# Kernel optimization log

Measured on AMD Instinct MI355X. Metric: run time of the kernel, lower is better.

## Reference

```python
import jax, jax.numpy as jnp
import numpy as np

EPS = 1e-06
SIGMA_C = 2.0


def setup_inputs() -> dict:
    key = jax.random.key(0)
    k1, k2 = jax.random.split(key)
    B, L, D, T = 16, 512, 256, 2048
    text = jax.random.normal(k1, (B, L, D), dtype=jnp.float32)
    durs = jax.random.randint(k2, (B, L), 0, 8, dtype=jnp.int64)
    return {"text": text, "durs": durs, "total_time": T}


def reference(text, durs, total_time):
    # text: [B, L, D], durs: [B, L] int, total_time: static python int T
    d = durs.astype(jnp.float32)
    # NOTE: faithful to original: mean = durs/2 + cumsum(durs) (cumsum includes current dur)
    mean = d / 2.0 + jnp.cumsum(d, axis=-1)            # [B, L]
    sigma = d / SIGMA_C + EPS                          # [B, L]
    t = jnp.arange(total_time, dtype=jnp.float32) + 0.5  # [T]
    # Normal pdf evaluated at t: exp(log_prob) = exp(-0.5 z^2) / (sigma * sqrt(2 pi))
    z = (t[None, :, None] - mean[:, None, :]) / sigma[:, None, :]  # [B, T, L]
    inv_norm = 1.0 / (sigma[:, None, :] * jnp.sqrt(2.0 * jnp.pi))
    probs = jnp.exp(-0.5 * z * z) * inv_norm           # [B, T, L]
    probs = probs / (probs.sum(-1, keepdims=True) + EPS)
    return jnp.einsum("btl,bld->btd", probs, text)     # [B, T, D]
```

## Files before the change

### kernel.cpp

```cpp
#include <hip/hip_runtime.h>
#include <math.h>

#define L 512
#define NTHREADS 256
#define BLOCK_TT 32
#define ZWIN 9.0f
#define NXCD 8

typedef __attribute__((ext_vector_type(8))) short bf16x8;
typedef __attribute__((ext_vector_type(4))) float f32x4;

static constexpr float EPS = 1e-6f;
static constexpr float INV_SQRT_2PI = 0.39894228040143267794f;

union BFrag { unsigned int u[4]; bf16x8 h; };

__global__ __launch_bounds__(NTHREADS, 4) void ge_mfma(
    const int*   __restrict__ durs,
    const float* __restrict__ text,
    float*       __restrict__ out,
    int B, int T, int tilesPerB, int nwg)
{
    __shared__ float2 s_mi[L];

    const int tid  = threadIdx.x;
    const int lane = tid & 63;
    const int wid  = tid >> 6;
    const int g    = lane >> 4;
    const int mrow = lane & 15;

    const int orig = blockIdx.x;
    const int wg   = (nwg % NXCD == 0) ? (orig & (NXCD - 1)) * (nwg / NXCD) + (orig >> 3)
                                       : orig;
    const int b      = wg / tilesPerB;
    const int tbase0 = (wg % tilesPerB) * BLOCK_TT;

    const int r0 = lane << 3;
    const int4 da = ((const int4*)(durs + (size_t)b * L + r0))[0];
    const int4 db = ((const int4*)(durs + (size_t)b * L + r0))[1];
    int dv[8] = {da.x, da.y, da.z, da.w, db.x, db.y, db.z, db.w};
    int cs[8];
    int run = 0;
    #pragma unroll
    for (int j = 0; j < 8; ++j) { run += dv[j]; cs[j] = run; }
    int v = run;
    #pragma unroll
    for (int off = 1; off < 64; off <<= 1) {
        int n = __shfl_up(v, off, 64);
        if (lane >= off) v += n;
    }
    const int excl = v - run;

    #pragma unroll
    for (int j = 0; j < 8; ++j) {
        const float d  = (float)dv[j];
        const float m  = (float)(cs[j] + excl) + 0.5f * d;
        const float sg = 0.5f * d + EPS;
        s_mi[r0 + j] = make_float2(m, 1.0f / sg);
    }
    asm volatile("s_waitcnt lgkmcnt(0)" ::: "memory");
    __builtin_amdgcn_sched_barrier(0);

    const float* tbp = text + (size_t)b * L * 256 + (wid << 6) + mrow;

    #pragma unroll
    for (int half = 0; half < 2; ++half) {
        const int t0 = tbase0 + (half << 4);

        const float tlo = (float)t0 + 0.5f, thi = (float)t0 + 15.5f;
        int mn = L, mx = -1;
        #pragma unroll
        for (int j = 0; j < 8; ++j) {
            const float d  = (float)dv[j];
            const float m  = (float)(cs[j] + excl) + 0.5f * d;
            const float sg = 0.5f * d + EPS;
            const float r  = ZWIN * sg;
            if (dv[j] >= 1 && m + r >= tlo && m - r <= thi) {
                mn = min(mn, r0 + j);
                mx = max(mx, r0 + j);
            }
        }
        #pragma unroll
        for (int off = 32; off > 0; off >>= 1) {
            mn = min(mn, __shfl_xor(mn, off, 64));
            mx = max(mx, __shfl_xor(mx, off, 64));
        }

        f32x4 acc0 = {0,0,0,0}, acc1 = {0,0,0,0}, acc2 = {0,0,0,0}, acc3 = {0,0,0,0};
        float psum = 0.f;
        const float tf = (float)(t0 + mrow) + 0.5f;

        for (int kb = (mn & ~7); kb <= mx; kb += 32) {
            const int k0 = kb + (g << 3);

            float p[8];
            #pragma unroll
            for (int j = 0; j < 8; ++j) {
                const int k = k0 + j;
                const float2 mi = s_mi[k & (L - 1)];
                const float u = (tf - mi.x) * mi.y;
                float pj = __expf(-0.5f * u * u) * mi.y * INV_SQRT_2PI;
                pj = (k <= mx) ? pj : 0.f;
                psum += pj;
                p[j] = pj;
            }
            BFrag A;
            #pragma unroll
            for (int w = 0; w < 4; ++w)
                asm("v_cvt_pk_bf16_f32 %0, %1, %2"
                    : "=v"(A.u[w]) : "v"(p[2 * w]), "v"(p[2 * w + 1]));

            BFrag B0, B1, B2, B3;
            #pragma unroll
            for (int jp = 0; jp < 4; ++jp) {
                const int ka = min(k0 + 2 * jp,     L - 1);
                const int kc = min(k0 + 2 * jp + 1, L - 1);
                const float* ra = tbp + (size_t)ka * 256;
                const float* rc = tbp + (size_t)kc * 256;
                const float a0 = ra[0], a1 = ra[16], a2 = ra[32], a3 = ra[48];
                const float c0 = rc[0], c1 = rc[16], c2 = rc[32], c3 = rc[48];
                asm("v_cvt_pk_bf16_f32 %0, %1, %2" : "=v"(B0.u[jp]) : "v"(a0), "v"(c0));
                asm("v_cvt_pk_bf16_f32 %0, %1, %2" : "=v"(B1.u[jp]) : "v"(a1), "v"(c1));
                asm("v_cvt_pk_bf16_f32 %0, %1, %2" : "=v"(B2.u[jp]) : "v"(a2), "v"(c2));
                asm("v_cvt_pk_bf16_f32 %0, %1, %2" : "=v"(B3.u[jp]) : "v"(a3), "v"(c3));
            }

            acc0 = __builtin_amdgcn_mfma_f32_16x16x32_bf16(A.h, B0.h, acc0, 0, 0, 0);
            acc1 = __builtin_amdgcn_mfma_f32_16x16x32_bf16(A.h, B1.h, acc1, 0, 0, 0);
            acc2 = __builtin_amdgcn_mfma_f32_16x16x32_bf16(A.h, B2.h, acc2, 0, 0, 0);
            acc3 = __builtin_amdgcn_mfma_f32_16x16x32_bf16(A.h, B3.h, acc3, 0, 0, 0);
        }

        psum += __shfl_xor(psum, 16, 64);
        psum += __shfl_xor(psum, 32, 64);
        const float rn = 1.0f / (psum + EPS);

        const int trow = g << 2;
        const float rr0 = __shfl(rn, trow + 0, 64);
        const float rr1 = __shfl(rn, trow + 1, 64);
        const float rr2 = __shfl(rn, trow + 2, 64);
        const float rr3 = __shfl(rn, trow + 3, 64);

        float* ob = out + ((size_t)b * T + t0 + trow) * 256 + (wid << 6) + mrow;
        if (t0 + trow + 3 < T) {
            ob[0*256 +  0] = acc0[0] * rr0;  ob[1*256 +  0] = acc0[1] * rr1;
            ob[2*256 +  0] = acc0[2] * rr2;  ob[3*256 +  0] = acc0[3] * rr3;
            ob[0*256 + 16] = acc1[0] * rr0;  ob[1*256 + 16] = acc1[1] * rr1;
            ob[2*256 + 16] = acc1[2] * rr2;  ob[3*256 + 16] = acc1[3] * rr3;
            ob[0*256 + 32] = acc2[0] * rr0;  ob[1*256 + 32] = acc2[1] * rr1;
            ob[2*256 + 32] = acc2[2] * rr2;  ob[3*256 + 32] = acc2[3] * rr3;
            ob[0*256 + 48] = acc3[0] * rr0;  ob[1*256 + 48] = acc3[1] * rr1;
            ob[2*256 + 48] = acc3[2] * rr2;  ob[3*256 + 48] = acc3[3] * rr3;
        }
    }
}

extern "C" void kernel_launch(void* const* d_in, const int* in_sizes, int n_in,
                              void* d_out, int out_size, void* d_ws, size_t ws_size,
                              hipStream_t stream) {
    const int*   durs = (const int*)d_in[1];
    const float* text = (const float*)d_in[0];
    float*       out  = (float*)d_out;

    const int BL = in_sizes[1];
    const int D  = in_sizes[0] / BL;
    const int B  = BL / L;
    const int T  = out_size / (B * D);
    const int tilesPerB = (T + BLOCK_TT - 1) / BLOCK_TT;
    const int nwg = B * tilesPerB;

    ge_mfma<<<dim3(nwg), dim3(NTHREADS), 0, stream>>>(durs, text, out, B, T, tilesPerB, nwg);
}
```

Before: 15.24 us.

## Merge the two 16-row halves into one K loop sharing text fragments

Instead of two separate K loops (one per 16-row half of the 32-row time tile), the kernel computes the active K window once for the whole tile and runs a single loop. Each iteration builds two probability fragments and reuses one set of loaded and converted text B fragments for 8 MFMAs. This halves the global loads and bf16 conversions of text per tile and removes a loop's overhead. In exchange it raises accumulator register pressure, and the K window is the union over both halves, so some extra zero-weight work is done.

Result: faster. 14.84 us (-2.6%).

```diff
diff --git a/kernel.cpp b/kernel.cpp
--- a/kernel.cpp
+++ b/kernel.cpp
@@ -51,106 +51,118 @@
     }
     const int excl = v - run;
 
+    const float tlo = (float)tbase0 + 0.5f;
+    const float thi = (float)tbase0 + (float)BLOCK_TT - 0.5f;
+    int mn = L, mx = -1;
     #pragma unroll
     for (int j = 0; j < 8; ++j) {
         const float d  = (float)dv[j];
         const float m  = (float)(cs[j] + excl) + 0.5f * d;
         const float sg = 0.5f * d + EPS;
         s_mi[r0 + j] = make_float2(m, 1.0f / sg);
+        const float r = ZWIN * sg;
+        if (dv[j] >= 1 && m + r >= tlo && m - r <= thi) {
+            mn = min(mn, r0 + j);
+            mx = max(mx, r0 + j);
+        }
+    }
+    #pragma unroll
+    for (int off = 32; off > 0; off >>= 1) {
+        mn = min(mn, __shfl_xor(mn, off, 64));
+        mx = max(mx, __shfl_xor(mx, off, 64));
     }
     asm volatile("s_waitcnt lgkmcnt(0)" ::: "memory");
     __builtin_amdgcn_sched_barrier(0);
 
+    f32x4 a00 = {0,0,0,0}, a01 = {0,0,0,0}, a02 = {0,0,0,0}, a03 = {0,0,0,0};
+    f32x4 a10 = {0,0,0,0}, a11 = {0,0,0,0}, a12 = {0,0,0,0}, a13 = {0,0,0,0};
+    float psum0 = 0.f, psum1 = 0.f;
+    const float tf0 = (float)(tbase0 + mrow) + 0.5f;
+    const float tf1 = tf0 + 16.f;
     const float* tbp = text + (size_t)b * L * 256 + (wid << 6) + mrow;
 
+    for (int kb = (mn & ~7); kb <= mx; kb += 32) {
+        const int k0 = kb + (g << 3);
+
+        BFrag A0, A1;
+        #pragma unroll
+        for (int jp = 0; jp < 4; ++jp) {
+            const int ka = k0 + 2 * jp;
+            const int kc = ka + 1;
+            const float2 mia = s_mi[ka & (L - 1)];
+            const float2 mic = s_mi[kc & (L - 1)];
+            const float ca = mia.y * INV_SQRT_2PI;
+            const float cc = mic.y * INV_SQRT_2PI;
+            const float u0a = (tf0 - mia.x) * mia.y;
+            const float u0c = (tf0 - mic.x) * mic.y;
+            const float u1a = (tf1 - mia.x) * mia.y;
+            const float u1c = (tf1 - mic.x) * mic.y;
+            float p0a = __expf(-0.5f * u0a * u0a) * ca;
+            float p0c = __expf(-0.5f * u0c * u0c) * cc;
+            float p1a = __expf(-0.5f * u1a * u1a) * ca;
+            float p1c = __expf(-0.5f * u1c * u1c) * cc;
+            p0a = (ka <= mx) ? p0a : 0.f;  p1a = (ka <= mx) ? p1a : 0.f;
+            p0c = (kc <= mx) ? p0c : 0.f;  p1c = (kc <= mx) ? p1c : 0.f;
+            psum0 += p0a + p0c;
+            psum1 += p1a + p1c;
+            asm("v_cvt_pk_bf16_f32 %0, %1, %2" : "=v"(A0.u[jp]) : "v"(p0a), "v"(p0c));
+            asm("v_cvt_pk_bf16_f32 %0, %1, %2" : "=v"(A1.u[jp]) : "v"(p1a), "v"(p1c));
+        }
+
+        BFrag B0, B1, B2, B3;
+        #pragma unroll
+        for (int jp = 0; jp < 4; ++jp) {
+            const int ka = min(k0 + 2 * jp,     L - 1);
+            const int kc = min(k0 + 2 * jp + 1, L - 1);
+            const float* ra = tbp + (size_t)ka * 256;
+            const float* rc = tbp + (size_t)kc * 256;
+            const float b0 = ra[0], b1 = ra[16], b2 = ra[32], b3 = ra[48];
+            const float c0 = rc[0], c1 = rc[16], c2 = rc[32], c3 = rc[48];
+            asm("v_cvt_pk_bf16_f32 %0, %1, %2" : "=v"(B0.u[jp]) : "v"(b0), "v"(c0));
+            asm("v_cvt_pk_bf16_f32 %0, %1, %2" : "=v"(B1.u[jp]) : "v"(b1), "v"(c1));
+            asm("v_cvt_pk_bf16_f32 %0, %1, %2" : "=v"(B2.u[jp]) : "v"(b2), "v"(c2));
+            asm("v_cvt_pk_bf16_f32 %0, %1, %2" : "=v"(B3.u[jp]) : "v"(b3), "v"(c3));
+        }
+
+        a00 = __builtin_amdgcn_mfma_f32_16x16x32_bf16(A0.h, B0.h, a00, 0, 0, 0);
+        a01 = __builtin_amdgcn_mfma_f32_16x16x32_bf16(A0.h, B1.h, a01, 0, 0, 0);
+        a02 = __builtin_amdgcn_mfma_f32_16x16x32_bf16(A0.h, B2.h, a02, 0, 0, 0);
+        a03 = __builtin_amdgcn_mfma_f32_16x16x32_bf16(A0.h, B3.h, a03, 0, 0, 0);
+        a10 = __builtin_amdgcn_mfma_f32_16x16x32_bf16(A1.h, B0.h, a10, 0, 0, 0);
+        a11 = __builtin_amdgcn_mfma_f32_16x16x32_bf16(A1.h, B1.h, a11, 0, 0, 0);
+        a12 = __builtin_amdgcn_mfma_f32_16x16x32_bf16(A1.h, B2.h, a12, 0, 0, 0);
+        a13 = __builtin_amdgcn_mfma_f32_16x16x32_bf16(A1.h, B3.h, a13, 0, 0, 0);
+    }
+
+    const int trow = g << 2;
     #pragma unroll
     for (int half = 0; half < 2; ++half) {
-        const int t0 = tbase0 + (half << 4);
+        float ps = half ? psum1 : psum0;
+        ps += __shfl_xor(ps, 16, 64);
+        ps += __shfl_xor(ps, 32, 64);
+        const float rn = 1.0f / (ps + EPS);
 
-        const float tlo = (float)t0 + 0.5f, thi = (float)t0 + 15.5f;
-        int mn = L, mx = -1;
-        #pragma unroll
-        for (int j = 0; j < 8; ++j) {
-            const float d  = (float)dv[j];
-            const float m  = (float)(cs[j] + excl) + 0.5f * d;
-            const float sg = 0.5f * d + EPS;
-            const float r  = ZWIN * sg;
-            if (dv[j] >= 1 && m + r >= tlo && m - r <= thi) {
-                mn = min(mn, r0 + j);
-                mx = max(mx, r0 + j);
-            }
-        }
-        #pragma unroll
-        for (int off = 32; off > 0; off >>= 1) {
-            mn = min(mn, __shfl_xor(mn, off, 64));
-            mx = max(mx, __shfl_xor(mx, off, 64));
-        }
-
-        f32x4 acc0 = {0,0,0,0}, acc1 = {0,0,0,0}, acc2 = {0,0,0,0}, acc3 = {0,0,0,0};
-        float psum = 0.f;
-        const float tf = (float)(t0 + mrow) + 0.5f;
-
-        for (int kb = (mn & ~7); kb <= mx; kb += 32) {
-            const int k0 = kb + (g << 3);
-
-            float p[8];
-            #pragma unroll
-            for (int j = 0; j < 8; ++j) {
-                const int k = k0 + j;
-                const float2 mi = s_mi[k & (L - 1)];
-                const float u = (tf - mi.x) * mi.y;
-                float pj = __expf(-0.5f * u * u) * mi.y * INV_SQRT_2PI;
-                pj = (k <= mx) ? pj : 0.f;
-                psum += pj;
-                p[j] = pj;
-            }
-            BFrag A;
-            #pragma unroll
-            for (int w = 0; w < 4; ++w)
-                asm("v_cvt_pk_bf16_f32 %0, %1, %2"
-                    : "=v"(A.u[w]) : "v"(p[2 * w]), "v"(p[2 * w + 1]));
-
-            BFrag B0, B1, B2, B3;
-            #pragma unroll
-            for (int jp = 0; jp < 4; ++jp) {
-                const int ka = min(k0 + 2 * jp,     L - 1);
-                const int kc = min(k0 + 2 * jp + 1, L - 1);
-                const float* ra = tbp + (size_t)ka * 256;
-                const float* rc = tbp + (size_t)kc * 256;
-                const float a0 = ra[0], a1 = ra[16], a2 = ra[32], a3 = ra[48];
-                const float c0 = rc[0], c1 = rc[16], c2 = rc[32], c3 = rc[48];
-                asm("v_cvt_pk_bf16_f32 %0, %1, %2" : "=v"(B0.u[jp]) : "v"(a0), "v"(c0));
-                asm("v_cvt_pk_bf16_f32 %0, %1, %2" : "=v"(B1.u[jp]) : "v"(a1), "v"(c1));
-                asm("v_cvt_pk_bf16_f32 %0, %1, %2" : "=v"(B2.u[jp]) : "v"(a2), "v"(c2));
-                asm("v_cvt_pk_bf16_f32 %0, %1, %2" : "=v"(B3.u[jp]) : "v"(a3), "v"(c3));
-            }
-
-            acc0 = __builtin_amdgcn_mfma_f32_16x16x32_bf16(A.h, B0.h, acc0, 0, 0, 0);
-            acc1 = __builtin_amdgcn_mfma_f32_16x16x32_bf16(A.h, B1.h, acc1, 0, 0, 0);
-            acc2 = __builtin_amdgcn_mfma_f32_16x16x32_bf16(A.h, B2.h, acc2, 0, 0, 0);
-            acc3 = __builtin_amdgcn_mfma_f32_16x16x32_bf16(A.h, B3.h, acc3, 0, 0, 0);
-        }
-
-        psum += __shfl_xor(psum, 16, 64);
-        psum += __shfl_xor(psum, 32, 64);
-        const float rn = 1.0f / (psum + EPS);
-
-        const int trow = g << 2;
         const float rr0 = __shfl(rn, trow + 0, 64);
         const float rr1 = __shfl(rn, trow + 1, 64);
         const float rr2 = __shfl(rn, trow + 2, 64);
         const float rr3 = __shfl(rn, trow + 3, 64);
 
+        const f32x4 c0 = half ? a10 : a00;
+        const f32x4 c1 = half ? a11 : a01;
+        const f32x4 c2 = half ? a12 : a02;
+        const f32x4 c3 = half ? a13 : a03;
+
+        const int t0 = tbase0 + (half << 4);
         float* ob = out + ((size_t)b * T + t0 + trow) * 256 + (wid << 6) + mrow;
         if (t0 + trow + 3 < T) {
-            ob[0*256 +  0] = acc0[0] * rr0;  ob[1*256 +  0] = acc0[1] * rr1;
-            ob[2*256 +  0] = acc0[2] * rr2;  ob[3*256 +  0] = acc0[3] * rr3;
-            ob[0*256 + 16] = acc1[0] * rr0;  ob[1*256 + 16] = acc1[1] * rr1;
-            ob[2*256 + 16] = acc1[2] * rr2;  ob[3*256 + 16] = acc1[3] * rr3;
-            ob[0*256 + 32] = acc2[0] * rr0;  ob[1*256 + 32] = acc2[1] * rr1;
-            ob[2*256 + 32] = acc2[2] * rr2;  ob[3*256 + 32] = acc2[3] * rr3;
-            ob[0*256 + 48] = acc3[0] * rr0;  ob[1*256 + 48] = acc3[1] * rr1;
-            ob[2*256 + 48] = acc3[2] * rr2;  ob[3*256 + 48] = acc3[3] * rr3;
+            ob[0*256 +  0] = c0[0] * rr0;  ob[1*256 +  0] = c0[1] * rr1;
+            ob[2*256 +  0] = c0[2] * rr2;  ob[3*256 +  0] = c0[3] * rr3;
+            ob[0*256 + 16] = c1[0] * rr0;  ob[1*256 + 16] = c1[1] * rr1;
+            ob[2*256 + 16] = c1[2] * rr2;  ob[3*256 + 16] = c1[3] * rr3;
+            ob[0*256 + 32] = c2[0] * rr0;  ob[1*256 + 32] = c2[1] * rr1;
+            ob[2*256 + 32] = c2[2] * rr2;  ob[3*256 + 32] = c2[3] * rr3;
+            ob[0*256 + 48] = c3[0] * rr0;  ob[1*256 + 48] = c3[1] * rr1;
+            ob[2*256 + 48] = c3[2] * rr2;  ob[3*256 + 48] = c3[3] * rr3;
         }
     }
 }
```
